# Optimization experiments

Measured on AMD Instinct MI355X. Metric: run time of the kernel, lower is better.

Reference implementation:

```python
import jax, jax.numpy as jnp
import numpy as np

DET = 512       # detector bins
N_THETA = 180   # projection angles, theta = 0..179 degrees (1 deg spacing)


def _ramp_filter(size):
    """skimage _get_fourier_filter(size, 'ramp'): spatial ramp -> FFT."""
    n = np.concatenate((np.arange(1, size // 2 + 1, 2),
                        np.arange(size // 2 - 1, 0, -2)))
    f = np.zeros(size)
    f[0] = 0.25
    f[1::2] = -1.0 / (np.pi * n) ** 2
    return jnp.asarray(2.0 * np.real(np.fft.fft(f)), dtype=jnp.float32)


def _iradon(x):
    B, C, det, A = x.shape
    theta = jnp.deg2rad(jnp.arange(A, dtype=jnp.float32))  # 0..179 deg

    # --- ramp filtering along the detector axis ---
    size = max(64, int(2 ** np.ceil(np.log2(2 * det))))  # 1024 for det=512
    filt = _ramp_filter(size)                            # (size,)
    xp = jnp.pad(x, ((0, 0), (0, 0), (0, size - det), (0, 0)))
    proj_f = jnp.fft.fft(xp, axis=2) * filt[None, None, :, None]
    filtered = jnp.real(jnp.fft.ifft(proj_f, axis=2))[:, :, :det, :]  # (B,C,det,A)

    # --- backprojection (circle=False) ---
    out_size = int(np.floor(np.sqrt(det ** 2 / 2.0)))  # 362
    radius = out_size // 2
    xpr = jnp.arange(out_size, dtype=jnp.float32)[:, None] - radius  # rows
    ypr = jnp.arange(out_size, dtype=jnp.float32)[None, :] - radius  # cols
    cos_t = jnp.cos(theta)
    sin_t = jnp.sin(theta)
    # detector coordinate for every (angle, pixel): t = y*cos - x*sin
    t = ypr[None] * cos_t[:, None, None] - xpr[None] * sin_t[:, None, None]  # (A,out,out)
    pos = t + det // 2          # index into detector axis (x = arange(det)-det//2)
    i0 = jnp.floor(pos).astype(jnp.int32)
    frac = pos - i0.astype(jnp.float32)
    in_range = ((pos >= 0) & (pos <= det - 1)).astype(jnp.float32)  # fill_value=0 outside
    i0c = jnp.clip(i0, 0, det - 1)
    i1c = jnp.clip(i0 + 1, 0, det - 1)

    P = out_size * out_size
    ft = jnp.moveaxis(filtered, 3, 2)                     # (B,C,A,det)
    idx0 = jnp.broadcast_to(i0c.reshape(A, P)[None, None], (B, C, A, P))
    idx1 = jnp.broadcast_to(i1c.reshape(A, P)[None, None], (B, C, A, P))
    g0 = jnp.take_along_axis(ft, idx0, axis=3)            # (B,C,A,P)
    g1 = jnp.take_along_axis(ft, idx1, axis=3)
    w = frac.reshape(A, P)[None, None]
    m = in_range.reshape(A, P)[None, None]
    val = ((1.0 - w) * g0 + w * g1) * m                   # bilinear-in-1D interp, 0 outside
    recon = val.sum(axis=2).reshape(B, C, out_size, out_size)
    return recon * (jnp.pi / (2.0 * A))


def setup_inputs() -> dict:
    key = jax.random.key(0)
    x = jax.random.normal(key, (4, 1, DET, N_THETA), dtype=jnp.float32)
    return {"x": x}


def reference(x):
    return _iradon(x)
```

## Files before the change

kernel.cpp:

```cpp
#include <hip/hip_runtime.h>
#include <math.h>

#define DET 512
#define NA  180
#define OUT 362
#define RAD 181

#define NSPLIT 6
#define APB    30
#define CHUNK  6
#define LSTRIDE 516

constexpr double PI_D = 3.14159265358979323846;

constexpr double tsin(double x) {
    double x2 = x * x;
    return x * (1.0 + x2 * (-1.0/6 + x2 * (1.0/120 + x2 * (-1.0/5040 +
               x2 * (1.0/362880 + x2 * (-1.0/39916800))))));
}
constexpr double tcos(double x) {
    double x2 = x * x;
    return 1.0 + x2 * (-0.5 + x2 * (1.0/24 + x2 * (-1.0/720 +
               x2 * (1.0/40320 + x2 * (-1.0/3628800)))));
}

struct Trig { float c[NA]; float s[NA]; };
constexpr Trig make_trig() {
    Trig t{};
    constexpr double r = PI_D / 180.0;
    for (int k = 0; k < NA; ++k) {
        double c, s;
        if (k <= 45)       { c =  tcos(k * r);          s =  tsin(k * r); }
        else if (k <= 90)  { c =  tsin((90 - k) * r);   s =  tcos((90 - k) * r); }
        else if (k <= 135) { c = -tsin((k - 90) * r);   s =  tcos((k - 90) * r); }
        else               { c = -tcos((180 - k) * r);  s =  tsin((180 - k) * r); }
        t.c[k] = (float)c; t.s[k] = (float)s;
    }
    return t;
}
__device__ constexpr Trig TRIG = make_trig();

struct WTbl { float w[DET / 2]; };
constexpr WTbl make_wt() {
    WTbl t{};
    for (int k = 0; k < DET / 2; ++k) {
        double m = (double)(2 * k + 1);
        t.w[k] = (float)(-2.0 / (PI_D * PI_D * m * m));
    }
    return t;
}
__device__ constexpr WTbl WTC = make_wt();

__global__ __launch_bounds__(512) void ramp_filter_kernel(
        const float* __restrict__ x, float* __restrict__ ft) {
    const int a = blockIdx.x;
    const int b = blockIdx.y;
    const int tid = threadIdx.x;

    __shared__ float xs[3 * DET];

    xs[tid]        = 0.0f;
    xs[1024 + tid] = 0.0f;
    xs[512 + tid]  = x[(b * DET + tid) * NA + a];
    __syncthreads();

    const float* p = xs + 512 + tid;
    float acc = 0.5f * p[0];
    #pragma unroll 4
    for (int k = 0; k < DET / 2; ++k) {
        int m = 2 * k + 1;
        acc = fmaf(WTC.w[k], p[-m] + p[m], acc);
    }
    ft[(b * NA + a) * DET + tid] = acc;
}

__device__ __forceinline__ float interp1(const float* __restrict__ L, float pos) {
    float pf = floorf(pos);
    int   i0 = (int)pf;
    float fr = pos - pf;
    float g0 = L[i0];
    float g1 = L[i0 + 1];
    float v  = fmaf(fr, g1 - g0, g0);
    return pos <= (float)(DET - 1) ? v : 0.0f;
}

__global__ __launch_bounds__(256, 8) void backproject_kernel(
        const float* __restrict__ ft, float* __restrict__ out) {
    const int bz = blockIdx.z;
    const int b  = bz / NSPLIT;
    const int sp = bz - b * NSPLIT;
    const int r0 = blockIdx.y * 32;
    const int c0 = blockIdx.x * 32;
    const int tid = threadIdx.x;
    const int tx = tid & 15;
    const int ty = tid >> 4;

    __shared__ float line[CHUNK * LSTRIDE];

    if (tid < CHUNK) line[tid * LSTRIDE + 512] = 0.0f;

    const float xpr = (float)(min(r0 + ty, OUT - 1) - RAD);
    const float ypr = (float)(min(c0 + tx, OUT - 1) - RAD);

    float a00 = 0.0f, a01 = 0.0f, a10 = 0.0f, a11 = 0.0f;

    const float* base = ft + (b * NA + sp * APB) * DET;

    for (int rd = 0; rd < APB / CHUNK; ++rd) {
        __syncthreads();
        const float4* g = (const float4*)(base + rd * CHUNK * DET);
        #pragma unroll
        for (int k = 0; k < (CHUNK * DET / 4) / 256; ++k) {
            int j4 = tid + k * 256;
            float4 v = g[j4];
            int c = j4 >> 7;
            int d = (j4 & 127) << 2;
            *(float4*)&line[c * LSTRIDE + d] = v;
        }
        __syncthreads();

        const int abase = sp * APB + rd * CHUNK;
        #pragma unroll
        for (int i = 0; i < CHUNK; ++i) {
            const float cv = TRIG.c[abase + i];
            const float sv = TRIG.s[abase + i];
            float p00 = fmaf(ypr, cv, fmaf(xpr, -sv, 256.0f));
            float p01 = fmaf(16.0f, cv, p00);
            float p10 = fmaf(-16.0f, sv, p00);
            float p11 = fmaf(-16.0f, sv, p01);
            const float* L = line + i * LSTRIDE;
            a00 += interp1(L, p00);
            a01 += interp1(L, p01);
            a10 += interp1(L, p10);
            a11 += interp1(L, p11);
        }
    }

    const float scale = (float)(PI_D / (2.0 * NA));
    const int r = r0 + ty;
    const int c = c0 + tx;
    float* ob = out + b * OUT * OUT;
    if (r < OUT) {
        if (c < OUT)      atomicAdd(&ob[r * OUT + c],      a00 * scale);
        if (c + 16 < OUT) atomicAdd(&ob[r * OUT + c + 16], a01 * scale);
    }
    if (r + 16 < OUT) {
        if (c < OUT)      atomicAdd(&ob[(r + 16) * OUT + c],      a10 * scale);
        if (c + 16 < OUT) atomicAdd(&ob[(r + 16) * OUT + c + 16], a11 * scale);
    }
}

extern "C" void kernel_launch(void* const* d_in, const int* in_sizes, int n_in,
                              void* d_out, int out_size, void* d_ws, size_t ws_size,
                              hipStream_t stream) {
    const float* x = (const float*)d_in[0];
    float* ft  = (float*)d_ws;
    float* out = (float*)d_out;

    const int B = in_sizes[0] / (DET * NA);

    hipMemsetAsync(out, 0, (size_t)out_size * sizeof(float), stream);
    ramp_filter_kernel<<<dim3(NA, B), 512, 0, stream>>>(x, ft);
    backproject_kernel<<<dim3((OUT + 31) / 32, (OUT + 31) / 32, B * NSPLIT),
                         256, 0, stream>>>(ft, out);
}
```

Measured before the change: 105.1 us.

## Register-block ramp filter so each thread computes eight detector outputs

```diff
diff --git a/kernel.cpp b/kernel.cpp
--- a/kernel.cpp
+++ b/kernel.cpp
@@ -40,38 +40,59 @@
 }
 __device__ constexpr Trig TRIG = make_trig();
 
-struct WTbl { float w[DET / 2]; };
-constexpr WTbl make_wt() {
-    WTbl t{};
-    for (int k = 0; k < DET / 2; ++k) {
-        double m = (double)(2 * k + 1);
-        t.w[k] = (float)(-2.0 / (PI_D * PI_D * m * m));
+#define GW_N 960
+struct GTbl { float g[GW_N]; };
+constexpr GTbl make_g() {
+    GTbl t{};
+    for (int m = 0; m < GW_N; ++m) {
+        if ((m & 1) && m <= 511) {
+            double md = (double)m;
+            t.g[m] = (float)(-2.0 / (PI_D * PI_D * md * md));
+        } else {
+            t.g[m] = 0.0f;
+        }
     }
     return t;
 }
-__device__ constexpr WTbl WTC = make_wt();
+__device__ constexpr GTbl GW = make_g();
 
-__global__ __launch_bounds__(512) void ramp_filter_kernel(
+__global__ __launch_bounds__(64) void ramp_filter_kernel(
         const float* __restrict__ x, float* __restrict__ ft) {
     const int a = blockIdx.x;
     const int b = blockIdx.y;
-    const int tid = threadIdx.x;
+    const int lane = threadIdx.x;
 
     __shared__ float xs[3 * DET];
 
-    xs[tid]        = 0.0f;
-    xs[1024 + tid] = 0.0f;
-    xs[512 + tid]  = x[(b * DET + tid) * NA + a];
+    #pragma unroll
+    for (int k = 0; k < DET / 64; ++k) {
+        int d = lane + 64 * k;
+        xs[d]        = 0.0f;
+        xs[1024 + d] = 0.0f;
+        xs[512 + d]  = x[(b * DET + d) * NA + a];
+    }
     __syncthreads();
 
-    const float* p = xs + 512 + tid;
-    float acc = 0.5f * p[0];
+    const float* p = xs + 512 + lane;
+
+    float acc[8];
+    #pragma unroll
+    for (int t = 0; t < 8; ++t) acc[t] = 0.5f * p[64 * t];
+
     #pragma unroll 4
-    for (int k = 0; k < DET / 2; ++k) {
-        int m = 2 * k + 1;
-        acc = fmaf(WTC.w[k], p[-m] + p[m], acc);
+    for (int jj = -511; jj <= 959; jj += 2) {
+        float v = p[jj];
+        #pragma unroll
+        for (int t = 0; t < 8; ++t) {
+            int m = jj - 64 * t;
+            m = m < 0 ? -m : m;
+            acc[t] = fmaf(GW.g[m], v, acc[t]);
+        }
     }
-    ft[(b * NA + a) * DET + tid] = acc;
+
+    float* o = ft + (b * NA + a) * DET + lane;
+    #pragma unroll
+    for (int t = 0; t < 8; ++t) o[64 * t] = acc[t];
 }
 
 __device__ __forceinline__ float interp1(const float* __restrict__ L, float pos) {
@@ -160,7 +181,7 @@
     const int B = in_sizes[0] / (DET * NA);
 
     hipMemsetAsync(out, 0, (size_t)out_size * sizeof(float), stream);
-    ramp_filter_kernel<<<dim3(NA, B), 512, 0, stream>>>(x, ft);
+    ramp_filter_kernel<<<dim3(NA, B), 64, 0, stream>>>(x, ft);
     backproject_kernel<<<dim3((OUT + 31) / 32, (OUT + 31) / 32, B * NSPLIT),
                          256, 0, stream>>>(ft, out);
 }
```

Result: slower. 199.7 us (+90.1%).

## Register-block ramp filter convolution with compile-time weights and split-K reduction

Applied to the files above, without the earlier changes.

```diff
diff --git a/kernel.cpp b/kernel.cpp
--- a/kernel.cpp
+++ b/kernel.cpp
@@ -40,38 +40,72 @@
 }
 __device__ constexpr Trig TRIG = make_trig();
 
-struct WTbl { float w[DET / 2]; };
-constexpr WTbl make_wt() {
-    WTbl t{};
-    for (int k = 0; k < DET / 2; ++k) {
-        double m = (double)(2 * k + 1);
-        t.w[k] = (float)(-2.0 / (PI_D * PI_D * m * m));
-    }
-    return t;
-}
-__device__ constexpr WTbl WTC = make_wt();
-
-__global__ __launch_bounds__(512) void ramp_filter_kernel(
+__host__ __device__ constexpr float rampw(int m) {
+    double md = (double)(m < 0 ? -m : m);
+    return (float)(-2.0 / (PI_D * PI_D * md * md));
+}
+
+__global__ __launch_bounds__(256) void ramp_filter_kernel(
         const float* __restrict__ x, float* __restrict__ ft) {
-    const int a = blockIdx.x;
-    const int b = blockIdx.y;
+    const int a   = blockIdx.x;
+    const int b   = blockIdx.y;
     const int tid = threadIdx.x;
+    const int t    = tid & 127;
+    const int half = tid >> 7;
+    const int q = (t & 31) + 128 * (t >> 5);
 
     __shared__ float xs[3 * DET];
+    __shared__ float red[4 * 128];
 
     xs[tid]        = 0.0f;
+    xs[256 + tid]  = 0.0f;
     xs[1024 + tid] = 0.0f;
+    xs[1280 + tid] = 0.0f;
     xs[512 + tid]  = x[(b * DET + tid) * NA + a];
+    xs[768 + tid]  = x[(b * DET + 256 + tid) * NA + a];
     __syncthreads();
 
-    const float* p = xs + 512 + tid;
-    float acc = 0.5f * p[0];
-    #pragma unroll 4
-    for (int k = 0; k < DET / 2; ++k) {
-        int m = 2 * k + 1;
-        acc = fmaf(WTC.w[k], p[-m] + p[m], acc);
-    }
-    ft[(b * NA + a) * DET + tid] = acc;
+    const float* p = xs + 512 + q;
+    float a0 = 0.0f, a1 = 0.0f, a2 = 0.0f, a3 = 0.0f;
+
+    if (half == 0) {
+        a0 = 0.5f * p[0];
+        a1 = 0.5f * p[32];
+        a2 = 0.5f * p[64];
+        a3 = 0.5f * p[96];
+        #pragma unroll
+        for (int k = 0; k < 280; ++k) {
+            const int r = -511 + 2 * k;
+            const float v = p[r];
+            if (r      >= -511 && r      <= 511) a0 = fmaf(rampw(r),      v, a0);
+            if (r - 32 >= -511 && r - 32 <= 511) a1 = fmaf(rampw(r - 32), v, a1);
+            if (r - 64 >= -511 && r - 64 <= 511) a2 = fmaf(rampw(r - 64), v, a2);
+            if (r - 96 >= -511 && r - 96 <= 511) a3 = fmaf(rampw(r - 96), v, a3);
+        }
+    } else {
+        #pragma unroll
+        for (int k = 0; k < 280; ++k) {
+            const int r = 49 + 2 * k;
+            const float v = p[r];
+            if (r      >= -511 && r      <= 511) a0 = fmaf(rampw(r),      v, a0);
+            if (r - 32 >= -511 && r - 32 <= 511) a1 = fmaf(rampw(r - 32), v, a1);
+            if (r - 64 >= -511 && r - 64 <= 511) a2 = fmaf(rampw(r - 64), v, a2);
+            if (r - 96 >= -511 && r - 96 <= 511) a3 = fmaf(rampw(r - 96), v, a3);
+        }
+        red[      t] = a0;
+        red[128 + t] = a1;
+        red[256 + t] = a2;
+        red[384 + t] = a3;
+    }
+    __syncthreads();
+
+    if (half == 0) {
+        float* o = ft + (b * NA + a) * DET + q;
+        o[0]  = a0 + red[      t];
+        o[32] = a1 + red[128 + t];
+        o[64] = a2 + red[256 + t];
+        o[96] = a3 + red[384 + t];
+    }
 }
 
 __device__ __forceinline__ float interp1(const float* __restrict__ L, float pos) {
@@ -160,7 +194,7 @@
     const int B = in_sizes[0] / (DET * NA);
 
     hipMemsetAsync(out, 0, (size_t)out_size * sizeof(float), stream);
-    ramp_filter_kernel<<<dim3(NA, B), 512, 0, stream>>>(x, ft);
+    ramp_filter_kernel<<<dim3(NA, B), 256, 0, stream>>>(x, ft);
     backproject_kernel<<<dim3((OUT + 31) / 32, (OUT + 31) / 32, B * NSPLIT),
                          256, 0, stream>>>(ft, out);
 }
```

After: 171.3 us. +63.0%, slower.
